# Kernel tuning notes

Measured on AMD Instinct MI355X. Metric: run time of the kernel, lower is better.

Reference implementation:

```python
import jax, jax.numpy as jnp
import numpy as np
import math

S = 72; IMG_W = 640; IMG_H = 360; STRIDE = 16
IN_CH = 256; AFC = 64
FMAP_H = IMG_H // STRIDE  # 22
FMAP_W = IMG_W // STRIDE  # 40
N_OFFSETS = S
LEFT_ANGLES = [72., 60., 49., 39., 30., 22.]
RIGHT_ANGLES = [108., 120., 131., 141., 150., 158.]
BOTTOM_ANGLES = [165., 150., 141., 131., 120., 108., 100., 90., 80., 72., 60., 49., 39., 30., 15.]
BATCH = 8


def _gen_anchor(start, angle, cut):
    n = FMAP_H if cut else N_OFFSETS
    ys = np.linspace(1., 0., n)
    a = np.zeros(5 + n)
    sx, sy = start
    a[2] = 1. - sy
    a[3] = sx
    a[5:] = (sx + (1. - ys - 1. + sy) / math.tan(angle * math.pi / 180.)) * IMG_W
    return a


def _gen_side(angles, nb, x=None, y=None):
    if x is None:
        starts = [(xx, y) for xx in np.linspace(1., 0., nb)]
    else:
        starts = [(x, yy) for yy in np.linspace(1., 0., nb)]
    anc = np.stack([_gen_anchor(s, a, False) for s in starts for a in angles])
    cut = np.stack([_gen_anchor(s, a, True) for s in starts for a in angles])
    return anc, cut


def build_anchor_tables():
    la, lc = _gen_side(LEFT_ANGLES, 72, x=0.)
    ra, rc = _gen_side(RIGHT_ANGLES, 72, x=1.)
    ba, bc = _gen_side(BOTTOM_ANGLES, 128, y=1.)
    anchors = np.concatenate([la, ba, ra]).astype(np.float32)  # [P, 5+S]
    cuts = np.concatenate([lc, bc, rc])                        # [P, 5+fmap_h]
    xs = np.flip(np.round(cuts[:, 5:] / STRIDE), axis=1).astype(np.int64)
    cut_xs = np.clip(xs, 0, FMAP_W - 1).astype(np.int32)       # [P, fmap_h]
    invalid = (xs < 0) | (xs > FMAP_W)                         # faithful to original (> not >=)
    return anchors, cut_xs, invalid


def setup_inputs():
    key = jax.random.key(0)
    ks = jax.random.split(key, 6)
    anchors, cut_xs, invalid = build_anchor_tables()
    P = anchors.shape[0]  # 2784
    D = AFC * FMAP_H      # 1408
    s = 0.02
    return {
        "x": jax.random.normal(ks[0], (BATCH, IN_CH, FMAP_H, FMAP_W), jnp.float32),
        "conv_w": jax.random.normal(ks[1], (AFC, IN_CH), jnp.float32) * s,
        "conv_b": jnp.zeros((AFC,), jnp.float32),
        "att_w": jax.random.normal(ks[2], (P - 1, D), jnp.float32) * s,
        "att_b": jnp.zeros((P - 1,), jnp.float32),
        "cls_w": jax.random.normal(ks[3], (2, 2 * D), jnp.float32) * s,
        "cls_b": jnp.zeros((2,), jnp.float32),
        "so_w": jax.random.normal(ks[4], (1, 2 * D), jnp.float32) * s,
        "so_b": jnp.zeros((1,), jnp.float32),
        "reg_w": jax.random.normal(ks[5], (N_OFFSETS + 1, 2 * D), jnp.float32) * s,
        "reg_b": jnp.zeros((N_OFFSETS + 1,), jnp.float32),
        "anchors": jnp.asarray(anchors),
        "cut_xs": jnp.asarray(cut_xs),
        "invalid_mask": jnp.asarray(invalid),
    }


def reference(x, conv_w, conv_b, att_w, att_b, cls_w, cls_b, so_w, so_b, reg_w, reg_b, anchors, cut_xs, invalid_mask):
    B = x.shape[0]
    P, H = cut_xs.shape
    # 1x1 conv
    feat = jnp.einsum('bchw,oc->bohw', x, conv_w) + conv_b[None, :, None, None]
    # fused anchor feature gather: rois[b,p,c,h] = feat[b,c,h,cut_xs[p,h]]
    rois = feat[:, :, jnp.arange(H)[None, :], cut_xs]           # [B,C,P,H]
    rois = jnp.transpose(rois, (0, 2, 1, 3))                    # [B,P,C,H]
    rois = jnp.where(invalid_mask[None, :, None, :], 0., rois)
    D = rois.shape[2] * H
    baf = rois.reshape(B, P, D)
    scores = baf.reshape(B * P, D) @ att_w.T + att_b
    attention = jax.nn.softmax(scores, axis=1).reshape(B, P, P - 1)
    # off-diagonal scatter (replaces torch eye/nonzero trick): M[b,i,j]=attention[b,i,j'] for j!=i, diag 0
    i_idx = jnp.arange(P)[:, None]
    j_off = jnp.arange(P - 1)[None, :]
    tgt_j = jnp.where(j_off < i_idx, j_off, j_off + 1)          # [P,P-1]
    M = jnp.zeros((B, P, P), x.dtype).at[:, jnp.broadcast_to(i_idx, (P, P - 1)), tgt_j].set(attention)
    # (baf^T @ M^T)^T == M @ baf
    att_feats = jnp.einsum('bpq,bqd->bpd', M, baf)
    feats = jnp.concatenate([att_feats, baf], axis=2).reshape(B * P, 2 * D)
    cls = (feats @ cls_w.T + cls_b).reshape(B, P, 2)
    so = jax.nn.sigmoid(feats @ so_w.T + so_b).reshape(B, P, 1)
    reg = (feats @ reg_w.T + reg_b).reshape(B, P, N_OFFSETS + 1)
    anc = jnp.broadcast_to(anchors[None], (B, P, anchors.shape[1]))
    reg_proposals = jnp.concatenate([cls, (anc[:, :, 2:3] + so) * 0.5, anc[:, :, 3:4], anc[:, :, 4:] + reg], axis=2)
    return reg_proposals, M, feat
```

## Files before the change

### kernel.cpp

```cpp
#include <hip/hip_runtime.h>
#include <stdint.h>

#define PTOT 2784
#define PM1  2783
#define DDIM 1408
#define NB   8
#define ROWS 22272
#define KHEAD 2816
#define MROW 2816
#define BTROWS 1536

typedef __attribute__((ext_vector_type(8))) short bf16x8;
typedef __attribute__((ext_vector_type(4))) float f32x4;
typedef long i64f8;

__device__ __forceinline__ short f2bf_rne(float x) {
    uint32_t u = __float_as_uint(x);
    u += 0x7fffu + ((u >> 16) & 1u);
    return (short)(u >> 16);
}

__device__ __forceinline__ unsigned char f2e4m3(float x) {
    uint32_t u = __float_as_uint(x);
    uint32_t sgn = (u >> 24) & 0x80u;
    uint32_t ax = u & 0x7fffffffu;
    ax += 0x7ffffu + ((ax >> 20) & 1u);
    if (ax >= 0x43E80000u) return (unsigned char)(sgn | 0x7Eu);
    if (ax < 0x3C800000u) return (unsigned char)sgn;
    uint32_t e = (ax >> 23) - 120u;
    uint32_t m = (ax >> 20) & 7u;
    return (unsigned char)(sgn | (e << 3) | m);
}

__device__ __forceinline__ void gld16(const void* g, void* l) {
    __builtin_amdgcn_global_load_lds(
        (const __attribute__((address_space(1))) void*)(uintptr_t)g,
        (__attribute__((address_space(3))) void*)(uint32_t)(uintptr_t)l,
        16, 0, 0);
}

__global__ __launch_bounds__(256) void k_conv(
    const float* __restrict__ x, const float* __restrict__ w,
    const float* __restrict__ cb, float* __restrict__ feat) {
  __shared__ float xs[256 * 32];
  int b = blockIdx.x / 28;
  int t0 = (blockIdx.x % 28) * 32;
  int t = threadIdx.x;
  for (int i = t; i < 256 * 32; i += 256) {
    int c = i >> 5, pos = i & 31;
    int hw = t0 + pos;
    xs[i] = (hw < 880) ? x[((size_t)b * 256 + c) * 880 + hw] : 0.f;
  }
  __syncthreads();
  int o = t & 63, g = t >> 6;
  float acc[8];
#pragma unroll
  for (int pp = 0; pp < 8; ++pp) acc[pp] = cb[o];
  const float* wr = w + o * 256;
  for (int c = 0; c < 256; ++c) {
    float wv = wr[c];
#pragma unroll
    for (int pp = 0; pp < 8; ++pp) acc[pp] += wv * xs[c * 32 + g + pp * 4];
  }
#pragma unroll
  for (int pp = 0; pp < 8; ++pp) {
    int hw = t0 + g + pp * 4;
    if (hw < 880) feat[((size_t)b * 64 + o) * 880 + hw] = acc[pp];
  }
}

__global__ __launch_bounds__(256) void k_prep(
    const float* __restrict__ att_w, const float* __restrict__ cls_w,
    const float* __restrict__ so_w, const float* __restrict__ reg_w,
    const float* __restrict__ cls_b, const float* __restrict__ so_b,
    const float* __restrict__ reg_b,
    short* __restrict__ attw, short* __restrict__ wbf,
    float* __restrict__ bias80, float* __restrict__ M,
    unsigned char* __restrict__ Mbf8, unsigned char* __restrict__ bafT8) {
  const int64_t n_attw = (int64_t)2816 * DDIM;
  const int64_t n_w = 80 * (int64_t)KHEAD;
  const int64_t n_pa = (int64_t)NB * MROW * 32;
  const int64_t n_pb = (int64_t)NB * BTROWS * 32;
  const int64_t total = n_attw + n_w + 80 + ROWS + n_pa + n_pb;
  for (int64_t i = (int64_t)blockIdx.x * 256 + threadIdx.x; i < total;
       i += (int64_t)gridDim.x * 256) {
    if (i < n_attw) {
      int j = (int)(i / DDIM), k = (int)(i - (int64_t)j * DDIM);
      float v = (j < PM1) ? att_w[(size_t)j * DDIM + k] : 0.f;
      attw[i] = f2bf_rne(v);
    } else if (i < n_attw + n_w) {
      int64_t ii = i - n_attw;
      int n = (int)(ii / KHEAD), k = (int)(ii - (int64_t)n * KHEAD);
      float v = 0.f;
      if (n < 2) v = cls_w[n * KHEAD + k];
      else if (n == 2) v = so_w[k];
      else if (n < 76) v = reg_w[(size_t)(n - 3) * KHEAD + k];
      wbf[ii] = f2bf_rne(v);
    } else if (i < n_attw + n_w + 80) {
      int n = (int)(i - n_attw - n_w);
      float v = 0.f;
      if (n < 2) v = cls_b[n];
      else if (n == 2) v = so_b[0];
      else if (n < 76) v = reg_b[n - 3];
      bias80[n] = v;
    } else if (i < n_attw + n_w + 80 + ROWS) {
      int r = (int)(i - n_attw - n_w - 80);
      int p = r % PTOT;
      M[(size_t)r * PTOT + p] = -1e30f;
    } else if (i < n_attw + n_w + 80 + ROWS + n_pa) {
      int64_t ii = i - n_attw - n_w - 80 - ROWS;
      int64_t row = ii >> 5; int c = (int)(ii & 31);
      Mbf8[row * 2816 + 2784 + c] = 0;
    } else {
      int64_t ii = i - n_attw - n_w - 80 - ROWS - n_pa;
      int64_t row = ii >> 5; int c = (int)(ii & 31);
      bafT8[row * 2816 + 2784 + c] = 0;
    }
  }
}

__global__ __launch_bounds__(256) void k_gather(
    const float* __restrict__ feat, const int* __restrict__ cutx,
    const unsigned char* __restrict__ inval,
    short* __restrict__ baf, unsigned char* __restrict__ bafT8) {
  int p0 = blockIdx.x * 64, d0 = blockIdx.y * 64, b = blockIdx.z;
  __shared__ short tile[64][72];
  int t = threadIdx.x;
  for (int i = t; i < 64 * 64; i += 256) {
    int pl = i >> 6, dl = i & 63;
    int p = p0 + pl, d = d0 + dl;
    float v = 0.f;
    if (p < PTOT && d < DDIM) {
      int c = d / 22, h = d - c * 22;
      if (!inval[p * 22 + h]) {
        int xc = cutx[p * 22 + h];
        v = feat[(((size_t)b * 64 + c) * 22 + h) * 40 + xc];
      }
    }
    tile[pl][dl] = f2bf_rne(v);
  }
  __syncthreads();
  if (d0 < DDIM) {
    for (int u = t; u < 512; u += 256) {
      int pl = u >> 3, dg = u & 7;
      int p = p0 + pl;
      if (p < PTOT) {
        bf16x8 v;
#pragma unroll
        for (int e = 0; e < 8; ++e) v[e] = tile[pl][dg * 8 + e];
        *(bf16x8*)&baf[((size_t)b * PTOT + p) * DDIM + d0 + dg * 8] = v;
      }
    }
  }
  for (int u = t; u < 512; u += 256) {
    int dl = u >> 3, pg = u & 7;
    int pbase = p0 + pg * 8;
    if (pbase + 7 < PTOT) {
      unsigned long long pk = 0;
#pragma unroll
      for (int e = 0; e < 8; ++e) {
        float fv = __uint_as_float((uint32_t)(unsigned short)tile[pg * 8 + e][dl] << 16);
        pk |= (unsigned long long)f2e4m3(fv) << (8 * e);
      }
      *(unsigned long long*)&bafT8[((size_t)b * BTROWS + d0 + dl) * 2816 + pbase] = pk;
    }
  }
}

__global__ __launch_bounds__(256) void k_scores(
    const short* __restrict__ baf, const short* __restrict__ attw,
    const float* __restrict__ att_b, float* __restrict__ Mout) {
  __shared__ char smA[8192];
  __shared__ char smB[8192];
  int wg = blockIdx.x;
  int xcd = wg & 7, lin = wg >> 3;
  int wgid = (xcd < 4) ? xcd * 479 + lin : 1916 + (xcd - 4) * 478 + lin;
  int it = wgid / 22, nt = wgid - it * 22;
  int m0 = it * 128, n0 = nt * 128;

  int t = threadIdx.x, w = t >> 6, l = t & 63;
  int lr = l & 15, lg = l >> 4;
  int wr = w >> 1, wc = w & 1;

  const char* gA[2]; const char* gB[2]; int dd[2];
#pragma unroll
  for (int c = 0; c < 2; ++c) {
    int o = w * 2048 + c * 1024 + l * 16;
    int row = o >> 6, col = o & 63;
    gA[c] = (const char*)(baf + (size_t)(m0 + row) * DDIM) + col;
    gB[c] = (const char*)(attw + (size_t)(n0 + row) * DDIM) + col;
    dd[c] = o;
  }

  f32x4 acc[4][4];
  const f32x4 fz = {0.f, 0.f, 0.f, 0.f};
#pragma unroll
  for (int mi = 0; mi < 4; ++mi)
#pragma unroll
    for (int ni = 0; ni < 4; ++ni) acc[mi][ni] = fz;

  const char* pA = smA + (wr * 64 + lr) * 64 + lg * 16;
  const char* pB = smB + (wc * 64 + lr) * 64 + lg * 16;

  for (int kt = 0; kt < 44; ++kt) {
    gld16(gA[0] + (size_t)kt * 64, smA + dd[0]);
    gld16(gA[1] + (size_t)kt * 64, smA + dd[1]);
    gld16(gB[0] + (size_t)kt * 64, smB + dd[0]);
    gld16(gB[1] + (size_t)kt * 64, smB + dd[1]);
    __syncthreads();
    bf16x8 av[4], bv[4];
#pragma unroll
    for (int i = 0; i < 4; ++i) av[i] = *(const bf16x8*)(pA + i * 1024);
#pragma unroll
    for (int i = 0; i < 4; ++i) bv[i] = *(const bf16x8*)(pB + i * 1024);
#pragma unroll
    for (int mi = 0; mi < 4; ++mi)
#pragma unroll
      for (int ni = 0; ni < 4; ++ni)
        acc[mi][ni] = __builtin_amdgcn_mfma_f32_16x16x32_bf16(
            av[mi], bv[ni], acc[mi][ni], 0, 0, 0);
    __syncthreads();
  }

#pragma unroll
  for (int mi = 0; mi < 4; ++mi) {
#pragma unroll
    for (int rg = 0; rg < 4; ++rg) {
      int gmi = m0 + wr * 64 + mi * 16 + lg * 4 + rg;
      int i = gmi % PTOT;
      float* Mrow = Mout + (size_t)gmi * PTOT;
#pragma unroll
      for (int ni = 0; ni < 4; ++ni) {
        int j = n0 + wc * 64 + ni * 16 + lr;
        if (j < PM1) {
          int q2 = j + (j >= i);
          Mrow[q2] = acc[mi][ni][rg] + att_b[j];
        }
      }
    }
  }
}

__global__ __launch_bounds__(256) void k_attfeat8(
    const unsigned char* __restrict__ Mbf8,
    const unsigned char* __restrict__ bafT8,
    short* __restrict__ attf) {
  __shared__ char smA[8192];
  __shared__ char smB[8192];
  int wg = blockIdx.x;
  int wgid = (wg & 7) * 242 + (wg >> 3);
  int bb = wgid / 242;
  int rem = wgid - bb * 242;
  int it = rem / 11, nt = rem - it * 11;
  int m0 = it * 128, n0 = nt * 128;
  const unsigned char* Ab = Mbf8 + ((size_t)bb * MROW + m0) * 2816;
  const unsigned char* Bb = bafT8 + ((size_t)bb * BTROWS + n0) * 2816;

  int t = threadIdx.x, w = t >> 6, l = t & 63;
  int lr = l & 15, lg = l >> 4;
  int wr = w >> 1, wc = w & 1;

  const char* gA[2]; const char* gB[2]; int dd[2];
#pragma unroll
  for (int c = 0; c < 2; ++c) {
    int o = c * 4096 + t * 16;
    int row = o >> 6;
    int colb = (o & 63) ^ (((o >> 7) & 3) << 4);
    gA[c] = (const char*)Ab + (size_t)row * 2816 + colb;
    gB[c] = (const char*)Bb + (size_t)row * 2816 + colb;
    dd[c] = o;
  }
  int offA[8], offB[8];
#pragma unroll
  for (int i = 0; i < 4; ++i) {
#pragma unroll
    for (int ks = 0; ks < 2; ++ks) {
      int xa = (wr * 64 + i * 16 + lr) * 64 + ks * 32 + lg * 8;
      offA[i * 2 + ks] = xa ^ (((xa >> 7) & 3) << 4);
      int xb = (wc * 64 + i * 16 + lr) * 64 + ks * 32 + lg * 8;
      offB[i * 2 + ks] = xb ^ (((xb >> 7) & 3) << 4);
    }
  }

  f32x4 acc[4][4];
  const f32x4 fz = {0.f, 0.f, 0.f, 0.f};
#pragma unroll
  for (int mi = 0; mi < 4; ++mi)
#pragma unroll
    for (int ni = 0; ni < 4; ++ni) acc[mi][ni] = fz;

  for (int kt = 0; kt < 44; ++kt) {
    gld16(gA[0] + (size_t)kt * 64, smA + dd[0]);
    gld16(gA[1] + (size_t)kt * 64, smA + dd[1]);
    gld16(gB[0] + (size_t)kt * 64, smB + dd[0]);
    gld16(gB[1] + (size_t)kt * 64, smB + dd[1]);
    __syncthreads();
#pragma unroll
    for (int ks = 0; ks < 2; ++ks) {
      i64f8 av[4], bv[4];
#pragma unroll
      for (int i = 0; i < 4; ++i) av[i] = *(const i64f8*)(smA + offA[i * 2 + ks]);
#pragma unroll
      for (int i = 0; i < 4; ++i) bv[i] = *(const i64f8*)(smB + offB[i * 2 + ks]);
#pragma unroll
      for (int mi = 0; mi < 4; ++mi)
#pragma unroll
        for (int ni = 0; ni < 4; ++ni)
          acc[mi][ni] = __builtin_amdgcn_mfma_f32_16x16x32_fp8_fp8(
              av[mi], bv[ni], acc[mi][ni], 0, 0, 0);
    }
    __syncthreads();
  }

  const float US = 1.0f / 1024.0f;
#pragma unroll
  for (int mi = 0; mi < 4; ++mi) {
#pragma unroll
    for (int rg = 0; rg < 4; ++rg) {
      int i = m0 + wr * 64 + mi * 16 + lg * 4 + rg;
      if (i < PTOT) {
        short* arow = attf + ((size_t)(bb * PTOT + i)) * DDIM + n0 + wc * 64;
#pragma unroll
        for (int ni = 0; ni < 4; ++ni)
          arow[ni * 16 + lr] = f2bf_rne(acc[mi][ni][rg] * US);
      }
    }
  }
}

__global__ __launch_bounds__(256) void k_softmax(float* __restrict__ M,
                                                 unsigned char* __restrict__ Mbf8) {
  __shared__ float red[8];
  int r = blockIdx.x;
  int b = r / PTOT, p = r - b * PTOT;
  float* pr = M + (size_t)r * PTOT;
  unsigned char* mb = Mbf8 + ((size_t)b * MROW + p) * 2816;
  int t = threadIdx.x;
  bool has2 = (t < 348 - 256);
  float v0[8], v1[8];
  f32x4 a0 = *(const f32x4*)(pr + t * 8);
  f32x4 a1 = *(const f32x4*)(pr + t * 8 + 4);
  float mx = -3.0e38f;
#pragma unroll
  for (int e = 0; e < 4; ++e) {
    v0[e] = a0[e]; v0[4 + e] = a1[e];
    mx = fmaxf(mx, fmaxf(v0[e], v0[4 + e]));
  }
  if (has2) {
    f32x4 b0 = *(const f32x4*)(pr + (256 + t) * 8);
    f32x4 b1 = *(const f32x4*)(pr + (256 + t) * 8 + 4);
#pragma unroll
    for (int e = 0; e < 4; ++e) {
      v1[e] = b0[e]; v1[4 + e] = b1[e];
      mx = fmaxf(mx, fmaxf(v1[e], v1[4 + e]));
    }
  }
#pragma unroll
  for (int off = 32; off; off >>= 1) mx = fmaxf(mx, __shfl_xor(mx, off));
  if ((t & 63) == 0) red[t >> 6] = mx;
  __syncthreads();
  mx = fmaxf(fmaxf(red[0], red[1]), fmaxf(red[2], red[3]));
  float s = 0.f;
#pragma unroll
  for (int e = 0; e < 8; ++e) { v0[e] = __expf(v0[e] - mx); s += v0[e]; }
  if (has2) {
#pragma unroll
    for (int e = 0; e < 8; ++e) { v1[e] = __expf(v1[e] - mx); s += v1[e]; }
  }
#pragma unroll
  for (int off = 32; off; off >>= 1) s += __shfl_xor(s, off);
  if ((t & 63) == 0) red[4 + (t >> 6)] = s;
  __syncthreads();
  s = (red[4] + red[5]) + (red[6] + red[7]);
  float inv = 1.f / s;
  float invs = inv * 1024.f;
  {
    f32x4 o0, o1; unsigned long long pk = 0;
#pragma unroll
    for (int e = 0; e < 8; ++e) {
      float wv = v0[e] * inv;
      if (e < 4) o0[e] = wv; else o1[e - 4] = wv;
      pk |= (unsigned long long)f2e4m3(v0[e] * invs) << (8 * e);
    }
    *(f32x4*)(pr + t * 8) = o0;
    *(f32x4*)(pr + t * 8 + 4) = o1;
    *(unsigned long long*)(mb + t * 8) = pk;
  }
  if (has2) {
    f32x4 o0, o1; unsigned long long pk = 0;
#pragma unroll
    for (int e = 0; e < 8; ++e) {
      float wv = v1[e] * inv;
      if (e < 4) o0[e] = wv; else o1[e - 4] = wv;
      pk |= (unsigned long long)f2e4m3(v1[e] * invs) << (8 * e);
    }
    *(f32x4*)(pr + (256 + t) * 8) = o0;
    *(f32x4*)(pr + (256 + t) * 8 + 4) = o1;
    *(unsigned long long*)(mb + (256 + t) * 8) = pk;
  }
}

__global__ __launch_bounds__(256) void k_head(
    const short* __restrict__ attf, const short* __restrict__ baf,
    const short* __restrict__ wbf, const float* __restrict__ bias80,
    const float* __restrict__ anch, float* __restrict__ out) {
  __shared__ short smA[64 * 32];
  __shared__ short smB[80 * 32];
  int r0 = blockIdx.x * 64;
  int t = threadIdx.x, wid = t >> 6, lane = t & 63;
  int rowa = t >> 2, kg = t & 3;
  const short* sA_att = attf + (size_t)(r0 + rowa) * DDIM + kg * 8;
  const short* sA_baf = baf + (size_t)(r0 + rowa) * DDIM + kg * 8;
  const short* sB0 = wbf + (size_t)rowa * KHEAD + kg * 8;
  const short* sB1 = wbf + (size_t)(64 + (t >> 2)) * KHEAD + (t & 3) * 8;
  char* lA = (char*)smA + wid * 1024;
  char* lB0 = (char*)smB + wid * 1024;
  char* lB1 = (char*)smB + 4096;
  int lr = lane & 15, lg = lane >> 4;
  const short* pA = smA + (wid * 16 + lr) * 32 + lg * 8;
  const short* pB = smB + lr * 32 + lg * 8;
  f32x4 acc[5];
  const f32x4 fz = {0.f, 0.f, 0.f, 0.f};
  for (int i2 = 0; i2 < 5; ++i2) acc[i2] = fz;
  for (int ks = 0; ks < 88; ++ks) {
    const short* sA = (ks < 44) ? (sA_att + ks * 32) : (sA_baf + (ks - 44) * 32);
    gld16(sA, lA);
    gld16(sB0 + ks * 32, lB0);
    if (t < 64) gld16(sB1 + ks * 32, lB1);
    __syncthreads();
    bf16x8 a = *(const bf16x8*)pA;
#pragma unroll
    for (int ni = 0; ni < 5; ++ni) {
      bf16x8 b = *(const bf16x8*)(pB + ni * 512);
      acc[ni] = __builtin_amdgcn_mfma_f32_16x16x32_bf16(a, b, acc[ni], 0, 0, 0);
    }
    __syncthreads();
  }
#pragma unroll
  for (int ni = 0; ni < 5; ++ni) {
#pragma unroll
    for (int rg = 0; rg < 4; ++rg) {
      int n = ni * 16 + lr;
      int i = wid * 16 + lg * 4 + rg;
      int rgl = r0 + i;
      int p = rgl % PTOT;
      float v = acc[ni][rg] + bias80[n];
      if (n < 2) {
        out[(size_t)rgl * 77 + n] = v;
      } else if (n == 2) {
        out[(size_t)rgl * 77 + 2] =
            (anch[(size_t)p * 77 + 2] + 1.f / (1.f + __expf(-v))) * 0.5f;
        out[(size_t)rgl * 77 + 3] = anch[(size_t)p * 77 + 3];
      } else if (n < 76) {
        out[(size_t)rgl * 77 + n + 1] = v + anch[(size_t)p * 77 + n + 1];
      }
    }
  }
}

extern "C" void kernel_launch(void* const* d_in, const int* in_sizes, int n_in,
                              void* d_out, int out_size, void* d_ws, size_t ws_size,
                              hipStream_t stream) {
  const float* x      = (const float*)d_in[0];
  const float* conv_w = (const float*)d_in[1];
  const float* conv_b = (const float*)d_in[2];
  const float* att_w  = (const float*)d_in[3];
  const float* att_b  = (const float*)d_in[4];
  const float* cls_w  = (const float*)d_in[5];
  const float* cls_b  = (const float*)d_in[6];
  const float* so_w   = (const float*)d_in[7];
  const float* so_b   = (const float*)d_in[8];
  const float* reg_w  = (const float*)d_in[9];
  const float* reg_b  = (const float*)d_in[10];
  const float* anchors= (const float*)d_in[11];
  const int*   cut_xs = (const int*)d_in[12];
  const unsigned char* invalid = (const unsigned char*)d_in[13];

  float* out_rp = (float*)d_out;
  float* Mmat = out_rp + (size_t)ROWS * 77;
  float* feat = Mmat + (size_t)ROWS * PTOT;

  char* wsp = (char*)d_ws;
  short* baf            = (short*)wsp;
  unsigned char* bafT8  = (unsigned char*)(wsp + 62717952ULL);
  unsigned char* Mbf8   = (unsigned char*)(wsp + 97320960ULL);
  short* attw           = (short*)(wsp + 160759808ULL);
  short* wbf            = (short*)(wsp + 168689664ULL);
  float* bias80         = (float*)(wsp + 169140224ULL);
  short* attf           = (short*)(wsp + 169140736ULL);

  k_conv<<<224, 256, 0, stream>>>(x, conv_w, conv_b, feat);
  k_prep<<<2048, 256, 0, stream>>>(att_w, cls_w, so_w, reg_w, cls_b, so_b, reg_b,
                                   attw, wbf, bias80, Mmat, Mbf8, bafT8);
  k_gather<<<dim3(44, 24, 8), 256, 0, stream>>>(feat, cut_xs, invalid, baf, bafT8);
  k_scores<<<3828, 256, 0, stream>>>(baf, attw, att_b, Mmat);
  k_softmax<<<ROWS, 256, 0, stream>>>(Mmat, Mbf8);
  k_attfeat8<<<1936, 256, 0, stream>>>(Mbf8, bafT8, attf);
  k_head<<<348, 256, 0, stream>>>(attf, baf, wbf, bias80, anchors, out_rp);
}
```

Before: 724.6 us.

## Store pre-softmax scores as bf16 scratch and swizzle LDS in score GEMM

When enough workspace is available, the score GEMM writes its logits as bf16 into a separate scratch buffer instead of fp32 into the output M, and softmax reads these bf16 values. This halves the score write and read traffic between the two kernels, at the cost of bf16 rounding of the logits before exp. The score GEMM also applies an XOR swizzle to its LDS tile layout to reduce bank conflicts on the fragment reads. The fast path depends on the workspace size exceeding a new threshold, and otherwise falls back to the old fp32 path.

```diff
diff --git a/kernel.cpp b/kernel.cpp
--- a/kernel.cpp
+++ b/kernel.cpp
@@ -18,6 +18,9 @@
     uint32_t u = __float_as_uint(x);
     u += 0x7fffu + ((u >> 16) & 1u);
     return (short)(u >> 16);
+}
+__device__ __forceinline__ float bf2f(short s) {
+    return __uint_as_float((uint32_t)(unsigned short)s << 16);
 }
 
 __device__ __forceinline__ unsigned char f2e4m3(float x) {
@@ -76,7 +79,8 @@
     const float* __restrict__ reg_b,
     short* __restrict__ attw, short* __restrict__ wbf,
     float* __restrict__ bias80, float* __restrict__ M,
-    unsigned char* __restrict__ Mbf8, unsigned char* __restrict__ bafT8) {
+    unsigned char* __restrict__ Mbf8, unsigned char* __restrict__ bafT8,
+    short* __restrict__ Msc) {
   const int64_t n_attw = (int64_t)2816 * DDIM;
   const int64_t n_w = 80 * (int64_t)KHEAD;
   const int64_t n_pa = (int64_t)NB * MROW * 32;
@@ -107,6 +111,7 @@
       int r = (int)(i - n_attw - n_w - 80);
       int p = r % PTOT;
       M[(size_t)r * PTOT + p] = -1e30f;
+      if (Msc) Msc[(size_t)r * PTOT + p] = f2bf_rne(-1e30f);
     } else if (i < n_attw + n_w + 80 + ROWS + n_pa) {
       int64_t ii = i - n_attw - n_w - 80 - ROWS;
       int64_t row = ii >> 5; int c = (int)(ii & 31);
@@ -159,7 +164,7 @@
       unsigned long long pk = 0;
 #pragma unroll
       for (int e = 0; e < 8; ++e) {
-        float fv = __uint_as_float((uint32_t)(unsigned short)tile[pg * 8 + e][dl] << 16);
+        float fv = bf2f(tile[pg * 8 + e][dl]);
         pk |= (unsigned long long)f2e4m3(fv) << (8 * e);
       }
       *(unsigned long long*)&bafT8[((size_t)b * BTROWS + d0 + dl) * 2816 + pbase] = pk;
@@ -167,9 +172,11 @@
   }
 }
 
+template<int OUTMODE>
 __global__ __launch_bounds__(256) void k_scores(
     const short* __restrict__ baf, const short* __restrict__ attw,
-    const float* __restrict__ att_b, float* __restrict__ Mout) {
+    const float* __restrict__ att_b, float* __restrict__ Mout,
+    short* __restrict__ Msc) {
   __shared__ char smA[8192];
   __shared__ char smB[8192];
   int wg = blockIdx.x;
@@ -186,10 +193,19 @@
 #pragma unroll
   for (int c = 0; c < 2; ++c) {
     int o = w * 2048 + c * 1024 + l * 16;
-    int row = o >> 6, col = o & 63;
-    gA[c] = (const char*)(baf + (size_t)(m0 + row) * DDIM) + col;
-    gB[c] = (const char*)(attw + (size_t)(n0 + row) * DDIM) + col;
+    int row = o >> 6;
+    int colb = (o & 63) ^ (((o >> 7) & 3) << 4);
+    gA[c] = (const char*)(baf + (size_t)(m0 + row) * DDIM) + colb;
+    gB[c] = (const char*)(attw + (size_t)(n0 + row) * DDIM) + colb;
     dd[c] = o;
+  }
+  int offA[4], offB[4];
+#pragma unroll
+  for (int i = 0; i < 4; ++i) {
+    int xa = (wr * 64 + i * 16 + lr) * 64 + lg * 16;
+    offA[i] = xa ^ (((xa >> 7) & 3) << 4);
+    int xb = (wc * 64 + i * 16 + lr) * 64 + lg * 16;
+    offB[i] = xb ^ (((xb >> 7) & 3) << 4);
   }
 
   f32x4 acc[4][4];
@@ -198,9 +214,6 @@
   for (int mi = 0; mi < 4; ++mi)
 #pragma unroll
     for (int ni = 0; ni < 4; ++ni) acc[mi][ni] = fz;
-
-  const char* pA = smA + (wr * 64 + lr) * 64 + lg * 16;
-  const char* pB = smB + (wc * 64 + lr) * 64 + lg * 16;
 
   for (int kt = 0; kt < 44; ++kt) {
     gld16(gA[0] + (size_t)kt * 64, smA + dd[0]);
@@ -210,9 +223,9 @@
     __syncthreads();
     bf16x8 av[4], bv[4];
 #pragma unroll
-    for (int i = 0; i < 4; ++i) av[i] = *(const bf16x8*)(pA + i * 1024);
-#pragma unroll
-    for (int i = 0; i < 4; ++i) bv[i] = *(const bf16x8*)(pB + i * 1024);
+    for (int i = 0; i < 4; ++i) av[i] = *(const bf16x8*)(smA + offA[i]);
+#pragma unroll
+    for (int i = 0; i < 4; ++i) bv[i] = *(const bf16x8*)(smB + offB[i]);
 #pragma unroll
     for (int mi = 0; mi < 4; ++mi)
 #pragma unroll
@@ -228,13 +241,14 @@
     for (int rg = 0; rg < 4; ++rg) {
       int gmi = m0 + wr * 64 + mi * 16 + lg * 4 + rg;
       int i = gmi % PTOT;
-      float* Mrow = Mout + (size_t)gmi * PTOT;
 #pragma unroll
       for (int ni = 0; ni < 4; ++ni) {
         int j = n0 + wc * 64 + ni * 16 + lr;
         if (j < PM1) {
           int q2 = j + (j >= i);
-          Mrow[q2] = acc[mi][ni][rg] + att_b[j];
+          float v = acc[mi][ni][rg] + att_b[j];
+          if (OUTMODE == 0) Mout[(size_t)gmi * PTOT + q2] = v;
+          else              Msc[(size_t)gmi * PTOT + q2] = f2bf_rne(v);
         }
       }
     }
@@ -328,32 +342,45 @@
   }
 }
 
+template<int INMODE>
 __global__ __launch_bounds__(256) void k_softmax(float* __restrict__ M,
-                                                 unsigned char* __restrict__ Mbf8) {
+                                                 unsigned char* __restrict__ Mbf8,
+                                                 const short* __restrict__ Msc) {
   __shared__ float red[8];
   int r = blockIdx.x;
   int b = r / PTOT, p = r - b * PTOT;
   float* pr = M + (size_t)r * PTOT;
+  const short* ms = INMODE ? (Msc + (size_t)r * PTOT) : (const short*)nullptr;
   unsigned char* mb = Mbf8 + ((size_t)b * MROW + p) * 2816;
   int t = threadIdx.x;
   bool has2 = (t < 348 - 256);
   float v0[8], v1[8];
-  f32x4 a0 = *(const f32x4*)(pr + t * 8);
-  f32x4 a1 = *(const f32x4*)(pr + t * 8 + 4);
   float mx = -3.0e38f;
-#pragma unroll
-  for (int e = 0; e < 4; ++e) {
-    v0[e] = a0[e]; v0[4 + e] = a1[e];
-    mx = fmaxf(mx, fmaxf(v0[e], v0[4 + e]));
-  }
+  if (INMODE == 0) {
+    f32x4 a0 = *(const f32x4*)(pr + t * 8);
+    f32x4 a1 = *(const f32x4*)(pr + t * 8 + 4);
+#pragma unroll
+    for (int e = 0; e < 4; ++e) { v0[e] = a0[e]; v0[4 + e] = a1[e]; }
+  } else {
+    bf16x8 a = *(const bf16x8*)(ms + t * 8);
+#pragma unroll
+    for (int e = 0; e < 8; ++e) v0[e] = bf2f(a[e]);
+  }
+#pragma unroll
+  for (int e = 0; e < 8; ++e) mx = fmaxf(mx, v0[e]);
   if (has2) {
-    f32x4 b0 = *(const f32x4*)(pr + (256 + t) * 8);
-    f32x4 b1 = *(const f32x4*)(pr + (256 + t) * 8 + 4);
-#pragma unroll
-    for (int e = 0; e < 4; ++e) {
-      v1[e] = b0[e]; v1[4 + e] = b1[e];
-      mx = fmaxf(mx, fmaxf(v1[e], v1[4 + e]));
-    }
+    if (INMODE == 0) {
+      f32x4 b0 = *(const f32x4*)(pr + (256 + t) * 8);
+      f32x4 b1 = *(const f32x4*)(pr + (256 + t) * 8 + 4);
+#pragma unroll
+      for (int e = 0; e < 4; ++e) { v1[e] = b0[e]; v1[4 + e] = b1[e]; }
+    } else {
+      bf16x8 bb = *(const bf16x8*)(ms + (256 + t) * 8);
+#pragma unroll
+      for (int e = 0; e < 8; ++e) v1[e] = bf2f(bb[e]);
+    }
+#pragma unroll
+    for (int e = 0; e < 8; ++e) mx = fmaxf(mx, v1[e]);
   }
 #pragma unroll
   for (int off = 32; off; off >>= 1) mx = fmaxf(mx, __shfl_xor(mx, off));
@@ -488,13 +515,23 @@
   short* wbf            = (short*)(wsp + 168689664ULL);
   float* bias80         = (float*)(wsp + 169140224ULL);
   short* attf           = (short*)(wsp + 169140736ULL);
+  short* Msc            = (short*)(wsp + 231858688ULL);
+  const size_t WS_FAST  = 231858688ULL + 124010496ULL;
+
+  bool fast = (ws_size >= WS_FAST);
 
   k_conv<<<224, 256, 0, stream>>>(x, conv_w, conv_b, feat);
   k_prep<<<2048, 256, 0, stream>>>(att_w, cls_w, so_w, reg_w, cls_b, so_b, reg_b,
-                                   attw, wbf, bias80, Mmat, Mbf8, bafT8);
+                                   attw, wbf, bias80, Mmat, Mbf8, bafT8,
+                                   fast ? Msc : (short*)nullptr);
   k_gather<<<dim3(44, 24, 8), 256, 0, stream>>>(feat, cut_xs, invalid, baf, bafT8);
-  k_scores<<<3828, 256, 0, stream>>>(baf, attw, att_b, Mmat);
-  k_softmax<<<ROWS, 256, 0, stream>>>(Mmat, Mbf8);
+  if (fast) {
+    k_scores<1><<<3828, 256, 0, stream>>>(baf, attw, att_b, (float*)nullptr, Msc);
+    k_softmax<1><<<ROWS, 256, 0, stream>>>(Mmat, Mbf8, Msc);
+  } else {
+    k_scores<0><<<3828, 256, 0, stream>>>(baf, attw, att_b, Mmat, (short*)nullptr);
+    k_softmax<0><<<ROWS, 256, 0, stream>>>(Mmat, Mbf8, (const short*)nullptr);
+  }
   k_attfeat8<<<1936, 256, 0, stream>>>(Mbf8, bafT8, attf);
   k_head<<<348, 256, 0, stream>>>(attf, baf, wbf, bias80, anchors, out_rp);
 }
```

Measured after the change: 705.1 us. 1.03x faster.
